# Kernel tuning notes

Hardware: AMD Instinct MI355X
Metric: run time of the kernel (lower is better)

The kernel has to match this reference:

```python
import jax, jax.numpy as jnp
from jax import lax
import numpy as np

B = 2
N_PER = 12000
TIMES = 16
C_IN = 4
# sparse_shape = grid_size[::-1] + [1,0,0], grid_size=[160,160,40]
S1 = (41, 160, 160)
S2 = (21, 80, 80)   # conv2: k3 s2 p1
S3 = (11, 40, 40)   # conv3: k3 s2 p1
S4 = (5, 20, 20)    # conv4: k3 s2 p(0,1,1)
SOUT = (2, 20, 20)  # conv_out: k(3,1,1) s(2,1,1) p0
# per-BN-layer channel counts, flattened into gamma/beta vectors
CH = [16, 16, 32, 32, 32, 64, 64, 64, 64, 64, 64, 128]
OFF = np.concatenate([[0], np.cumsum(CH)]).tolist()


def _downsample_coords(coords, in_shape, k, s, p):
    # spconv SparseConv3d output index rule: output j active iff some active
    # input x satisfies j*s - p <= x <= j*s - p + k - 1 within bounds.
    out_shape = np.array([(in_shape[i] + 2 * p[i] - k[i]) // s[i] + 1 for i in range(3)])
    b, xs = coords[:, :1], coords[:, 1:]
    s_arr = np.array(s)
    cand = []
    for o0 in range(k[0]):
        for o1 in range(k[1]):
            for o2 in range(k[2]):
                j = xs + np.array([p[0] - o0, p[1] - o1, p[2] - o2])
                ok = np.all(j % s_arr == 0, axis=1)
                jj = j // s_arr
                ok &= np.all((jj >= 0) & (jj < out_shape), axis=1)
                cand.append(np.concatenate([b[ok], jj[ok]], axis=1))
    return np.unique(np.concatenate(cand, axis=0), axis=0).astype(np.int32)


def _make_coords():
    rng = np.random.default_rng(0)
    ncell = S1[0] * S1[1] * S1[2]
    per = []
    for b in range(B):
        flat = rng.choice(ncell, size=N_PER, replace=False)
        z, y, x = np.unravel_index(flat, S1)
        per.append(np.stack([np.full(N_PER, b), z, y, x], axis=1))
    c1 = np.concatenate(per, axis=0).astype(np.int32)
    c2 = _downsample_coords(c1, S1, (3, 3, 3), (2, 2, 2), (1, 1, 1))
    c3 = _downsample_coords(c2, S2, (3, 3, 3), (2, 2, 2), (1, 1, 1))
    c4 = _downsample_coords(c3, S3, (3, 3, 3), (2, 2, 2), (0, 1, 1))
    c5 = _downsample_coords(c4, S4, (3, 1, 1), (2, 1, 1), (0, 0, 0))
    return c1, c2, c3, c4, c5


def _w(key, shape):
    fan_in = shape[0] * shape[1] * shape[2] * shape[3]
    return jax.random.normal(key, shape, jnp.float32) * np.float32(np.sqrt(2.0 / fan_in))


def setup_inputs():
    c1, c2, c3, c4, c5 = _make_coords()
    ks = jax.random.split(jax.random.key(0), 16)
    t = TIMES
    return {
        "voxel_features": jax.random.normal(ks[0], (c1.shape[0], C_IN), jnp.float32),
        "w_in": _w(ks[1], (3, 3, 3, C_IN, t)),
        "w1": _w(ks[2], (3, 3, 3, t, t)),
        "w2_0": _w(ks[3], (3, 3, 3, t, 2 * t)),
        "w2_1": _w(ks[4], (3, 3, 3, 2 * t, 2 * t)),
        "w2_2": _w(ks[5], (3, 3, 3, 2 * t, 2 * t)),
        "w3_0": _w(ks[6], (3, 3, 3, 2 * t, 4 * t)),
        "w3_1": _w(ks[7], (3, 3, 3, 4 * t, 4 * t)),
        "w3_2": _w(ks[8], (3, 3, 3, 4 * t, 4 * t)),
        "w4_0": _w(ks[9], (3, 3, 3, 4 * t, 4 * t)),
        "w4_1": _w(ks[10], (3, 3, 3, 4 * t, 4 * t)),
        "w4_2": _w(ks[11], (3, 3, 3, 4 * t, 4 * t)),
        "w_out": _w(ks[12], (3, 1, 1, 4 * t, 8 * t)),
        "gamma": 1.0 + 0.1 * jax.random.normal(ks[13], (sum(CH),), jnp.float32),
        "beta": 0.1 * jax.random.normal(ks[14], (sum(CH),), jnp.float32),
        "coords1": jnp.asarray(c1), "coords2": jnp.asarray(c2),
        "coords3": jnp.asarray(c3), "coords4": jnp.asarray(c4),
        "coords_out": jnp.asarray(c5),
    }


def _sp_conv(feats, in_coords, w, in_shape, out_coords, stride, padding):
    # spconv's rulebook gather->matmul->scatter over active sites computes the
    # same values as a dense conv on a zero-filled grid, read back only at the
    # active output coordinates (subm: out_coords == in_coords).
    dense = jnp.zeros((B,) + in_shape + (feats.shape[1],), feats.dtype)
    dense = dense.at[in_coords[:, 0], in_coords[:, 1], in_coords[:, 2], in_coords[:, 3]].set(feats)
    out = lax.conv_general_dilated(dense, w, window_strides=stride,
                                   padding=[(p, p) for p in padding],
                                   dimension_numbers=("NDHWC", "DHWIO", "NDHWC"))
    return out[out_coords[:, 0], out_coords[:, 1], out_coords[:, 2], out_coords[:, 3]]


def _bn_relu(x, g, b):
    # nn.BatchNorm1d(eps=1e-3) in training mode over the active voxels, + ReLU
    mu = jnp.mean(x, axis=0)
    var = jnp.mean(jnp.square(x - mu), axis=0)
    return jax.nn.relu((x - mu) * (g * lax.rsqrt(var + 1e-3)) + b)


def _forward(voxel_features, ws, gamma, beta, c1, c2, c3, c4, c5):
    layers = [
        (0, c1, S1, c1, (1, 1, 1), (1, 1, 1)),   # conv_input (subm, 4->16)
        (1, c1, S1, c1, (1, 1, 1), (1, 1, 1)),   # conv1 (subm)
        (2, c1, S1, c2, (2, 2, 2), (1, 1, 1)),   # conv2 spconv s2
        (3, c2, S2, c2, (1, 1, 1), (1, 1, 1)),
        (4, c2, S2, c2, (1, 1, 1), (1, 1, 1)),
        (5, c2, S2, c3, (2, 2, 2), (1, 1, 1)),   # conv3 spconv s2
        (6, c3, S3, c3, (1, 1, 1), (1, 1, 1)),
        (7, c3, S3, c3, (1, 1, 1), (1, 1, 1)),
        (8, c3, S3, c4, (2, 2, 2), (0, 1, 1)),   # conv4 spconv s2, pad (0,1,1)
        (9, c4, S4, c4, (1, 1, 1), (1, 1, 1)),
        (10, c4, S4, c4, (1, 1, 1), (1, 1, 1)),
        (11, c4, S4, c5, (2, 1, 1), (0, 0, 0)),  # conv_out k(3,1,1) s(2,1,1)
    ]
    x = voxel_features
    for i, ci, si, co, st, pd in layers:
        x = _sp_conv(x, ci, ws[i], si, co, st, pd)
        x = _bn_relu(x, gamma[OFF[i]:OFF[i + 1]], beta[OFF[i]:OFF[i + 1]])
    return x  # encoded_spconv_tensor features, [N_out, 8*times]


def reference(voxel_features, w_in, w1, w2_0, w2_1, w2_2, w3_0, w3_1, w3_2,
              w4_0, w4_1, w4_2, w_out, gamma, beta,
              coords1, coords2, coords3, coords4, coords_out):
    ws = [w_in, w1, w2_0, w2_1, w2_2, w3_0, w3_1, w3_2, w4_0, w4_1, w4_2, w_out]
    return _forward(voxel_features, ws, gamma, beta,
                    coords1, coords2, coords3, coords4, coords_out)
```

## Files before the change

kernel.cpp:

```cpp
#include <hip/hip_runtime.h>
#include <hip/hip_bf16.h>


typedef __attribute__((ext_vector_type(8))) short bf16x8;
typedef __attribute__((ext_vector_type(4))) short bf16x4s;
typedef __attribute__((ext_vector_type(4))) float f32x4;

typedef const __attribute__((address_space(1))) unsigned int* gas_ptr;
typedef __attribute__((address_space(3))) unsigned int* las_ptr;

__device__ __forceinline__ void dma16(const unsigned short* g, unsigned short* l) {
    __builtin_amdgcn_global_load_lds((gas_ptr)g, (las_ptr)l, 16, 0, 0);
}

__device__ inline unsigned short f2bf(float f) {
    unsigned u = __builtin_bit_cast(unsigned, f);
    u += 0x7FFFu + ((u >> 16) & 1u);
    return (unsigned short)(u >> 16);
}

struct ScatterArgs {
    const int* coords[4];
    int* grid[4];
    int n[4];
    int D[4], H[4], W[4];
};

__global__ __launch_bounds__(256) void scatter_grid_all(ScatterArgs a) {
    const int l = blockIdx.y;
    const int i = blockIdx.x * 256 + threadIdx.x;
    if (i >= a.n[l]) return;
    const int* c = a.coords[l] + 4 * i;
    a.grid[l][((c[0] * a.D[l] + c[1]) * a.H[l] + c[2]) * a.W[l] + c[3]] = i;
}

struct PrepArgs {
    const float* src[11];
    unsigned short* dst[11];
    int T[11], CIN[11], COUT[11], total[11];
};

__global__ __launch_bounds__(256) void prep_w_all(PrepArgs a) {
    const int l = blockIdx.y;
    const int i = blockIdx.x * 256 + threadIdx.x;
    if (i >= a.total[l]) return;
    const int COUT = a.COUT[l], CIN = a.CIN[l], T = a.T[l];
    const int co = i % COUT; const int r = i / COUT; const int ci = r % CIN; const int t = r / CIN;
    unsigned short v = (t < T) ? f2bf(a.src[l][i]) : (unsigned short)0;
    a.dst[l][((size_t)t * COUT + co) * CIN + ci] = v;
}

__global__ __launch_bounds__(256, 4) void sp_conv0(const float* __restrict__ fin,
                                                   const int* __restrict__ grid,
                                                   const int* __restrict__ oc, int n_out,
                                                   const float* __restrict__ w,
                                                   float* __restrict__ out,
                                                   int D, int H, int W) {
    const int c = threadIdx.x & 15;
    const int p = (blockIdx.x * 256 + threadIdx.x) >> 4;
    if (p >= n_out) return;
    const int b   = oc[4*p+0];
    const int iz0 = oc[4*p+1] - 1;
    const int iy0 = oc[4*p+2] - 1;
    const int ix0 = oc[4*p+3] - 1;
    const int* gb = grid + b * (D * H * W);
    float acc = 0.f;
    for (int kd = 0; kd < 3; ++kd) {
        const int iz = iz0 + kd;
        if ((unsigned)iz >= (unsigned)D) continue;
        for (int kh = 0; kh < 3; ++kh) {
            const int iy = iy0 + kh;
            if ((unsigned)iy >= (unsigned)H) continue;
            for (int kw = 0; kw < 3; ++kw) {
                const int ix = ix0 + kw;
                if ((unsigned)ix >= (unsigned)W) continue;
                const int idx = gb[(iz*H + iy)*W + ix];
                if (idx < 0) continue;
                const float4 v = *(const float4*)(fin + (size_t)idx * 4);
                const float* wp = w + (size_t)((kd*3 + kh)*3 + kw) * 64 + c;
                acc = fmaf(v.x, wp[0],  acc);
                acc = fmaf(v.y, wp[16], acc);
                acc = fmaf(v.z, wp[32], acc);
                acc = fmaf(v.w, wp[48], acc);
            }
        }
    }
    out[(size_t)p*16 + c] = acc;
}

template<int COUT, int BT>
__global__ __launch_bounds__(256, 4) void sp_conv_lds16(
    const unsigned short* __restrict__ fin, const int* __restrict__ grid,
    const int* __restrict__ oc, int n_out,
    const unsigned short* __restrict__ wt, float* __restrict__ out,
    float* __restrict__ stats,
    int D, int H, int W, int sz, int sy, int sx, int pz, int py, int px)
{
    constexpr int T  = 27;
    constexpr int NBATCH = (T + BT - 1)/BT;
    constexpr int TP = NBATCH*BT;
    constexpr int NT = COUT/16;
    constexpr int NB = (COUT == 16) ? BT/2 : BT;

    __shared__ unsigned short Abuf[4*BT*16*16];
    __shared__ unsigned short Bbuf[BT*COUT*16];
    __shared__ float ls[2*COUT];

    const int l     = threadIdx.x & 63;
    const int w     = threadIdx.x >> 6;
    const int n     = l & 15;
    const int quad  = l >> 4;
    const int pbase = blockIdx.x * 64 + w * 16;

    if (threadIdx.x < 2*COUT) ls[threadIdx.x] = 0.f;

    int idx[TP];
    if (quad == 0) {
        int pc = pbase + n;
        if (pc > n_out - 1) pc = n_out - 1;
        const int4 cc = ((const int4*)oc)[pc];
        const int* gb = grid + cc.x * (D * H * W);
        const int iz0 = cc.y * sz - pz;
        const int iy0 = cc.z * sy - py;
        const int ix0 = cc.w * sx - px;
#pragma unroll
        for (int tap = 0; tap < TP; ++tap) {
            const int te = tap < T ? tap : 0;
            const int kd = te/9, kr = te%9, kh = kr/3, kw = kr%3;
            const int iz = iz0 + kd, iy = iy0 + kh, ix = ix0 + kw;
            const bool ok = (tap < T) && (unsigned)iz < (unsigned)D &&
                            (unsigned)iy < (unsigned)H && (unsigned)ix < (unsigned)W;
            const int cz = iz < 0 ? 0 : (iz >= D ? D-1 : iz);
            const int cy = iy < 0 ? 0 : (iy >= H ? H-1 : iy);
            const int cx = ix < 0 ? 0 : (ix >= W ? W-1 : ix);
            const int g = gb[(cz*H + cy)*W + cx];
            idx[tap] = ok ? g : -1;
        }
    }

    f32x4 acc[NT];
#pragma unroll
    for (int t = 0; t < NT; ++t) acc[t] = (f32x4){0.f, 0.f, 0.f, 0.f};

    const int h  = l >> 5;
    const int m  = (l >> 1) & 15;
    const int ch = l & 1;

#pragma unroll
    for (int tb0 = 0; tb0 < TP; tb0 += BT) {
#pragma unroll
        for (int q = 0; q < BT/2; ++q) {
            const int v0 = __shfl(idx[tb0 + 2*q],     m);
            const int v1 = __shfl(idx[tb0 + 2*q + 1], m);
            const int row = h ? v1 : v0;
            const unsigned short* gp = fin + (ptrdiff_t)row*16 + ch*8;
            unsigned short* lp = Abuf + (w*BT + 2*q)*16*16;
            dma16(gp, lp);
        }
        for (int q = w; q < NB; q += 4) {
            if constexpr (COUT == 16) {
                const int tap = tb0 + 2*q + h;
                const int tw = tap < T ? tap : T;
                const unsigned short* gp = wt + ((size_t)tw*COUT + m)*16 + ch*8;
                unsigned short* lp = Bbuf + (2*q)*COUT*16;
                dma16(gp, lp);
            } else {
                const int tap = tb0 + q;
                const int tw = tap < T ? tap : T;
                const int r = l >> 1;
                const unsigned short* gp = wt + ((size_t)tw*COUT + r)*16 + ch*8;
                unsigned short* lp = Bbuf + q*COUT*16;
                dma16(gp, lp);
            }
        }
        __syncthreads();
#pragma unroll
        for (int jp = 0; jp < BT/2; ++jp) {
            const int ts = 2*jp + (quad >> 1);
            bf16x8 a = *(const bf16x8*)(Abuf + ((w*BT + ts)*16 + n)*16 + (quad & 1)*8);
#pragma unroll
            for (int t = 0; t < NT; ++t) {
                bf16x8 b = *(const bf16x8*)(Bbuf + (ts*COUT + t*16 + n)*16 + (quad & 1)*8);
                acc[t] = __builtin_amdgcn_mfma_f32_16x16x32_bf16(a, b, acc[t], 0, 0, 0);
            }
        }
        __syncthreads();
    }

#pragma unroll
    for (int t = 0; t < NT; ++t)
#pragma unroll
        for (int r = 0; r < 4; ++r) {
            const int p = pbase + quad*4 + r;
            if (p < n_out) out[(size_t)p * COUT + t*16 + n] = acc[t][r];
        }

#pragma unroll
    for (int t = 0; t < NT; ++t) {
        float s1 = 0.f, s2 = 0.f;
#pragma unroll
        for (int r = 0; r < 4; ++r) {
            const int p = pbase + quad*4 + r;
            if (p < n_out) { const float v = acc[t][r]; s1 += v; s2 += v*v; }
        }
        s1 += __shfl_xor(s1, 16); s2 += __shfl_xor(s2, 16);
        s1 += __shfl_xor(s1, 32); s2 += __shfl_xor(s2, 32);
        if (quad == 0) {
            atomicAdd(&ls[t*16 + n], s1);
            atomicAdd(&ls[COUT + t*16 + n], s2);
        }
    }
    __syncthreads();
    if (threadIdx.x < 2*COUT) atomicAdd(&stats[threadIdx.x], ls[threadIdx.x]);
}

template<int CIN, int COUT, int BT, int KD, int KH, int KW, int MB>
__global__ __launch_bounds__(256, MB) void sp_conv_lds(
    const unsigned short* __restrict__ fin, const int* __restrict__ grid,
    const int* __restrict__ oc, int n_out,
    const unsigned short* __restrict__ wt, float* __restrict__ out,
    float* __restrict__ stats,
    int D, int H, int W, int sz, int sy, int sx, int pz, int py, int px)
{
    constexpr int T    = KD*KH*KW;
    constexpr int NBATCH = (T + BT - 1)/BT;
    constexpr int TP   = NBATCH*BT;
    constexpr int NT   = COUT/16;
    constexpr int S    = CIN/32;
    constexpr int LPR  = CIN/8;
    constexpr int RPD  = 64/LPR;
    constexpr int ADMA = 16/RPD;
    constexpr int BDMA = COUT/RPD;

    __shared__ unsigned short Abuf[4*BT*16*CIN];
    __shared__ unsigned short Bbuf[BT*COUT*CIN];
    __shared__ float ls[2*COUT];

    const int l     = threadIdx.x & 63;
    const int w     = threadIdx.x >> 6;
    const int n     = l & 15;
    const int quad  = l >> 4;
    const int pbase = blockIdx.x * 64 + w * 16;

    if (threadIdx.x < 2*COUT) ls[threadIdx.x] = 0.f;

    int idx[TP];
    if (quad == 0) {
        int pc = pbase + n;
        if (pc > n_out - 1) pc = n_out - 1;
        const int4 cc = ((const int4*)oc)[pc];
        const int* gb = grid + cc.x * (D * H * W);
        const int iz0 = cc.y * sz - pz;
        const int iy0 = cc.z * sy - py;
        const int ix0 = cc.w * sx - px;
#pragma unroll
        for (int tap = 0; tap < TP; ++tap) {
            const int te = tap < T ? tap : 0;
            const int kd = te/(KH*KW), kr = te%(KH*KW), kh = kr/KW, kw = kr%KW;
            const int iz = iz0 + kd, iy = iy0 + kh, ix = ix0 + kw;
            const bool ok = (tap < T) && (unsigned)iz < (unsigned)D &&
                            (unsigned)iy < (unsigned)H && (unsigned)ix < (unsigned)W;
            const int cz = iz < 0 ? 0 : (iz >= D ? D-1 : iz);
            const int cy = iy < 0 ? 0 : (iy >= H ? H-1 : iy);
            const int cx = ix < 0 ? 0 : (ix >= W ? W-1 : ix);
            const int g = gb[(cz*H + cy)*W + cx];
            idx[tap] = ok ? g : -1;
        }
    }

    f32x4 acc[NT];
#pragma unroll
    for (int t = 0; t < NT; ++t) acc[t] = (f32x4){0.f, 0.f, 0.f, 0.f};

#pragma unroll
    for (int tb0 = 0; tb0 < TP; tb0 += BT) {
#pragma unroll
        for (int j = 0; j < BT; ++j) {
#pragma unroll
            for (int d = 0; d < ADMA; ++d) {
                const int m  = d*RPD + l/LPR;
                const int i0 = __shfl(idx[tb0+j], m);
                const int slot = (l % LPR) ^ (m % LPR);
                const unsigned short* gp = fin + (ptrdiff_t)i0*CIN + slot*8;
                unsigned short* lp = Abuf + ((w*BT + j)*16 + d*RPD)*CIN;
                dma16(gp, lp);
            }
        }
        for (int q = w; q < BT*BDMA; q += 4) {
            const int j = q / BDMA, d = q % BDMA;
            const int t = tb0 + j;
            const int tw = t < T ? t : T;
            const int r  = d*RPD + l/LPR;
            const int slot = (l % LPR) ^ (r % LPR);
            const unsigned short* gp = wt + ((size_t)tw*COUT + r)*CIN + slot*8;
            unsigned short* lp = Bbuf + (j*COUT + d*RPD)*CIN;
            dma16(gp, lp);
        }
        __syncthreads();
#pragma unroll
        for (int j = 0; j < BT; ++j) {
            const unsigned short* Aw = Abuf + (w*BT + j)*16*CIN;
            const unsigned short* Bw = Bbuf + j*COUT*CIN;
#pragma unroll
            for (int s = 0; s < S; ++s) {
                const int c = s*4 + quad;
                bf16x8 a = *(const bf16x8*)(Aw + n*CIN + ((c ^ (n % LPR)) * 8));
#pragma unroll
                for (int t = 0; t < NT; ++t) {
                    const int r = t*16 + n;
                    bf16x8 b = *(const bf16x8*)(Bw + r*CIN + ((c ^ (r % LPR)) * 8));
                    acc[t] = __builtin_amdgcn_mfma_f32_16x16x32_bf16(a, b, acc[t], 0, 0, 0);
                }
            }
        }
        __syncthreads();
    }

#pragma unroll
    for (int t = 0; t < NT; ++t)
#pragma unroll
        for (int r = 0; r < 4; ++r) {
            const int p = pbase + quad*4 + r;
            if (p < n_out) out[(size_t)p * COUT + t*16 + n] = acc[t][r];
        }

#pragma unroll
    for (int t = 0; t < NT; ++t) {
        float s1 = 0.f, s2 = 0.f;
#pragma unroll
        for (int r = 0; r < 4; ++r) {
            const int p = pbase + quad*4 + r;
            if (p < n_out) { const float v = acc[t][r]; s1 += v; s2 += v*v; }
        }
        s1 += __shfl_xor(s1, 16); s2 += __shfl_xor(s2, 16);
        s1 += __shfl_xor(s1, 32); s2 += __shfl_xor(s2, 32);
        if (quad == 0) {
            atomicAdd(&ls[t*16 + n], s1);
            atomicAdd(&ls[COUT + t*16 + n], s2);
        }
    }
    __syncthreads();
    if (threadIdx.x < 2*COUT) atomicAdd(&stats[threadIdx.x], ls[threadIdx.x]);
}

template<int C>
__global__ __launch_bounds__(256) void reduce_stats(const float* __restrict__ x, int nn,
                                                    float* __restrict__ stats)
{
    constexpr int R = 256 / C;
    __shared__ float s1[256];
    __shared__ float s2[256];
    const int c = threadIdx.x % C;
    const int r = threadIdx.x / C;
    float a1 = 0.f, a2 = 0.f;
    for (int i = blockIdx.x * R + r; i < nn; i += R * gridDim.x) {
        float v = x[(size_t)i*C + c];
        a1 += v;
        a2 += v * v;
    }
    s1[threadIdx.x] = a1;
    s2[threadIdx.x] = a2;
    __syncthreads();
    for (int off = 128; off >= C; off >>= 1) {
        if (threadIdx.x < off) {
            s1[threadIdx.x] += s1[threadIdx.x + off];
            s2[threadIdx.x] += s2[threadIdx.x + off];
        }
        __syncthreads();
    }
    if (threadIdx.x < C) {
        atomicAdd(&stats[c],     s1[threadIdx.x]);
        atomicAdd(&stats[C + c], s2[threadIdx.x]);
    }
}

__device__ inline void stv4(float* p, float4 v) { *(float4*)p = v; }
__device__ inline void stv4(unsigned short* p, float4 v) {
    bf16x4s o;
    o.x = (short)f2bf(v.x); o.y = (short)f2bf(v.y);
    o.z = (short)f2bf(v.z); o.w = (short)f2bf(v.w);
    *(bf16x4s*)p = o;
}

template<int C, typename OUT>
__global__ __launch_bounds__(256) void bn_relu_apply(const float* __restrict__ x,
                                                     OUT* __restrict__ y, int nn,
                                                     const float* __restrict__ stats,
                                                     const float* __restrict__ gamma,
                                                     const float* __restrict__ beta)
{
    const size_t q = (size_t)blockIdx.x * blockDim.x + threadIdx.x;
    if (q >= (size_t)nn * (C/4)) return;
    const int c = (int)(q % (size_t)(C/4)) * 4;
    const float inv_n = 1.f / (float)nn;
    const float4 xv = *(const float4*)(x + q*4);
    const float4 s1 = *(const float4*)(stats + c);
    const float4 s2 = *(const float4*)(stats + C + c);
    const float4 gm = *(const float4*)(gamma + c);
    const float4 bt = *(const float4*)(beta + c);
    float4 o;
    { float mu=s1.x*inv_n, var=s2.x*inv_n-mu*mu, g=gm.x*rsqrtf(var+1e-3f);
      float v=(xv.x-mu)*g+bt.x; o.x = v>0.f? v:0.f; }
    { float mu=s1.y*inv_n, var=s2.y*inv_n-mu*mu, g=gm.y*rsqrtf(var+1e-3f);
      float v=(xv.y-mu)*g+bt.y; o.y = v>0.f? v:0.f; }
    { float mu=s1.z*inv_n, var=s2.z*inv_n-mu*mu, g=gm.z*rsqrtf(var+1e-3f);
      float v=(xv.z-mu)*g+bt.z; o.z = v>0.f? v:0.f; }
    { float mu=s1.w*inv_n, var=s2.w*inv_n-mu*mu, g=gm.w*rsqrtf(var+1e-3f);
      float v=(xv.w-mu)*g+bt.w; o.w = v>0.f? v:0.f; }
    stv4(y + q*4, o);
}

extern "C" void kernel_launch(void* const* d_in, const int* in_sizes, int n_in,
                              void* d_out, int out_size, void* d_ws, size_t ws_size,
                              hipStream_t stream) {
    const float* WPTR[12] = {
        (const float*)d_in[1], (const float*)d_in[2], (const float*)d_in[3],
        (const float*)d_in[4], (const float*)d_in[5], (const float*)d_in[6],
        (const float*)d_in[7], (const float*)d_in[8], (const float*)d_in[9],
        (const float*)d_in[10], (const float*)d_in[11], (const float*)d_in[12] };
    const float* vf    = (const float*)d_in[0];
    const float* gamma = (const float*)d_in[13];
    const float* beta  = (const float*)d_in[14];
    const int* c1 = (const int*)d_in[15];
    const int* c2 = (const int*)d_in[16];
    const int* c3 = (const int*)d_in[17];
    const int* c4 = (const int*)d_in[18];
    const int* c5 = (const int*)d_in[19];
    const int N1 = in_sizes[15] / 4;
    const int N2 = in_sizes[16] / 4;
    const int N3 = in_sizes[17] / 4;
    const int N4 = in_sizes[18] / 4;
    const int N5 = in_sizes[19] / 4;

    static const int LT[12]  = {27,27,27,27,27,27,27,27,27,27,27,3};
    static const int LCI[12] = {4,16,16,32,32,32,64,64,64,64,64,64};
    static const int LCO[12] = {16,16,32,32,32,64,64,64,64,64,64,128};

    const size_t G1 = (size_t)2*41*160*160;
    const size_t G2 = (size_t)2*21*80*80;
    const size_t G3 = (size_t)2*11*40*40;
    const size_t G4 = (size_t)2*5*20*20;
    int* grid1 = (int*)d_ws;
    int* grid2 = grid1 + G1;
    int* grid3 = grid2 + G2;
    int* grid4 = grid3 + G3;
    float* stats = (float*)(grid4 + G4);

    size_t maxE = (size_t)N1*16;
    if ((size_t)N2*32  > maxE) maxE = (size_t)N2*32;
    if ((size_t)N3*64  > maxE) maxE = (size_t)N3*64;
    if ((size_t)N4*64  > maxE) maxE = (size_t)N4*64;
    if ((size_t)N5*128 > maxE) maxE = (size_t)N5*128;
    maxE = (maxE + 7) & ~(size_t)7;

    float* raw = stats + 12*256;
    unsigned short* padA = (unsigned short*)(raw + maxE);
    unsigned short* fA   = padA + 128;
    unsigned short* padB = fA + maxE;
    unsigned short* fB   = padB + 128;
    unsigned short* wtb  = fB + maxE;
    size_t wtoff[12];
    {
        size_t o = 0;
        for (int i = 1; i < 12; ++i) {
            wtoff[i] = o;
            o += (size_t)(LT[i] + 1) * LCI[i] * LCO[i];
        }
    }

    hipMemsetAsync(grid1, 0xFF, (G1+G2+G3+G4)*sizeof(int), stream);
    hipMemsetAsync(stats, 0, 12*256*sizeof(float), stream);
    hipMemsetAsync(padA, 0, 128*sizeof(unsigned short), stream);
    hipMemsetAsync(padB, 0, 128*sizeof(unsigned short), stream);

    {
        ScatterArgs sa;
        sa.coords[0]=c1; sa.coords[1]=c2; sa.coords[2]=c3; sa.coords[3]=c4;
        sa.grid[0]=grid1; sa.grid[1]=grid2; sa.grid[2]=grid3; sa.grid[3]=grid4;
        sa.n[0]=N1; sa.n[1]=N2; sa.n[2]=N3; sa.n[3]=N4;
        sa.D[0]=41; sa.H[0]=160; sa.W[0]=160;
        sa.D[1]=21; sa.H[1]= 80; sa.W[1]= 80;
        sa.D[2]=11; sa.H[2]= 40; sa.W[2]= 40;
        sa.D[3]= 5; sa.H[3]= 20; sa.W[3]= 20;
        int mx = N1; if (N2>mx) mx=N2; if (N3>mx) mx=N3; if (N4>mx) mx=N4;
        dim3 g((mx + 255)/256, 4);
        scatter_grid_all<<<g, 256, 0, stream>>>(sa);
    }
    {
        PrepArgs pa;
        int mx = 0;
        for (int i = 1; i < 12; ++i) {
            pa.src[i-1] = WPTR[i];
            pa.dst[i-1] = wtb + wtoff[i];
            pa.T[i-1] = LT[i]; pa.CIN[i-1] = LCI[i]; pa.COUT[i-1] = LCO[i];
            pa.total[i-1] = (LT[i]+1)*LCI[i]*LCO[i];
            if (pa.total[i-1] > mx) mx = pa.total[i-1];
        }
        dim3 g((mx + 255)/256, 11);
        prep_w_all<<<g, 256, 0, stream>>>(pa);
    }

    enum { GOFF_0 = 0, GOFF_1 = 16, GOFF_2 = 32, GOFF_3 = 64, GOFF_4 = 96, GOFF_5 = 128,
           GOFF_6 = 192, GOFF_7 = 256, GOFF_8 = 320, GOFF_9 = 384, GOFF_10 = 448, GOFF_11 = 512 };

#define APPLY(i, COUT, NP, FOUT_T, FOUT) \
    bn_relu_apply<COUT, FOUT_T><<<(((size_t)(NP)*(COUT)/4) + 255)/256, 256, 0, stream>>>( \
        raw, FOUT, NP, stats + (i)*256, gamma + GOFF_##i, beta + GOFF_##i);

    sp_conv0<<<((size_t)N1*16 + 255)/256, 256, 0, stream>>>(vf, grid1, c1, N1, WPTR[0], raw, 41,160,160);
    { int rb = (N1 + 15)/16; if (rb > 240) rb = 240;
      reduce_stats<16><<<rb, 256, 0, stream>>>(raw, N1, stats + 0*256); }
    APPLY(0, 16, N1, unsigned short, fA);

#define CONVS(i, COUT, BT, FIN, GRD, OC, NP, D,H,W, SZ,SY,SX, PZ,PY,PX) \
    sp_conv_lds16<COUT,BT><<<((NP)+63)/64, 256, 0, stream>>>( \
        FIN, GRD, OC, NP, wtb + wtoff[i], raw, stats + (i)*256, D,H,W, SZ,SY,SX, PZ,PY,PX);

#define CONVL(i, CIN, COUT, BT, MB, KD,KH,KW, FIN, GRD, OC, NP, D,H,W, SZ,SY,SX, PZ,PY,PX) \
    sp_conv_lds<CIN,COUT,BT,KD,KH,KW,MB><<<((NP)+63)/64, 256, 0, stream>>>( \
        FIN, GRD, OC, NP, wtb + wtoff[i], raw, stats + (i)*256, D,H,W, SZ,SY,SX, PZ,PY,PX);

    CONVS( 1, 16, 10,   fA, grid1, c1, N1, 41,160,160, 1,1,1, 1,1,1); APPLY( 1, 16, N1, unsigned short, fB);
    CONVS( 2, 32, 10,   fB, grid1, c2, N2, 41,160,160, 2,2,2, 1,1,1); APPLY( 2, 32, N2, unsigned short, fA);
    CONVL ( 3, 32, 32, 9, 2, 3,3,3, fA, grid2, c2, N2, 21, 80, 80, 1,1,1, 1,1,1); APPLY( 3, 32, N2, unsigned short, fB);
    CONVL ( 4, 32, 32, 9, 2, 3,3,3, fB, grid2, c2, N2, 21, 80, 80, 1,1,1, 1,1,1); APPLY( 4, 32, N2, unsigned short, fA);
    CONVL ( 5, 32, 64, 9, 2, 3,3,3, fA, grid2, c3, N3, 21, 80, 80, 2,2,2, 1,1,1); APPLY( 5, 64, N3, unsigned short, fB);
    CONVL ( 6, 64, 64, 9, 1, 3,3,3, fB, grid3, c3, N3, 11, 40, 40, 1,1,1, 1,1,1); APPLY( 6, 64, N3, unsigned short, fA);
    CONVL ( 7, 64, 64, 9, 1, 3,3,3, fA, grid3, c3, N3, 11, 40, 40, 1,1,1, 1,1,1); APPLY( 7, 64, N3, unsigned short, fB);
    CONVL ( 8, 64, 64, 9, 1, 3,3,3, fB, grid3, c4, N4, 11, 40, 40, 2,2,2, 0,1,1); APPLY( 8, 64, N4, unsigned short, fA);
    CONVL ( 9, 64, 64, 9, 1, 3,3,3, fA, grid4, c4, N4,  5, 20, 20, 1,1,1, 1,1,1); APPLY( 9, 64, N4, unsigned short, fB);
    CONVL (10, 64, 64, 9, 1, 3,3,3, fB, grid4, c4, N4,  5, 20, 20, 1,1,1, 1,1,1); APPLY(10, 64, N4, unsigned short, fA);
    CONVL (11, 64,128, 3, 2, 3,1,1, fA, grid4, c5, N5,  5, 20, 20, 2,1,1, 0,0,0); APPLY(11, 128, N5, float, (float*)d_out);
#undef CONVS
#undef CONVL
#undef APPLY
}
```

Measured before the change: 431.2 us.

## Run submanifold convs as dense tiled convolutions over a scattered bf16 grid

Adds a dense-grid path for the stride-1 submanifold convolutions at levels 2-4. BN+ReLU now scatters activations into a zeroed dense bf16 volume. A new kernel then loads a haloed 3D tile into LDS and runs all 27 taps as MFMAs on contiguous rows, writing results only at active sites. This replaces the per-voxel gather through the index grid with regular tile loads. The cost is extra memsets of the dense volume and wasted MFMA work on empty cells, which is significant given how sparse the levels are.

```diff
diff --git a/kernel.cpp b/kernel.cpp
--- a/kernel.cpp
+++ b/kernel.cpp
@@ -343,6 +343,158 @@
     if (threadIdx.x < 2*COUT) atomicAdd(&stats[threadIdx.x], ls[threadIdx.x]);
 }
 
+template<int C, int TZ, int TY, int TX, int BTW>
+__global__ __launch_bounds__(256, 1) void sp_conv_dense(
+    const unsigned short* __restrict__ dense, const int* __restrict__ grid,
+    const unsigned short* __restrict__ wt, float* __restrict__ out,
+    float* __restrict__ stats, const unsigned short* __restrict__ zrow,
+    int D, int H, int W, int ZTn, int YTn, int XTn)
+{
+    constexpr int T   = 27;
+    constexpr int HZ = TZ+2, HY = TY+2, HX = TX+2;
+    constexpr int R   = HZ*HY*HX;
+    constexpr int LPR = C/8;
+    constexpr int RPD = 64/LPR;
+    constexpr int RPI = 4*RPD;
+    constexpr int NDMA = (R + RPI - 1)/RPI;
+    constexpr int RPAD = NDMA*RPI;
+    constexpr int M   = TZ*TY*TX;
+    constexpr int WPW = M/4;
+    constexpr int MT  = WPW/16;
+    constexpr int NT  = C/16;
+    constexpr int S   = C/32;
+    constexpr int BDMA = C/RPD;
+
+    __shared__ unsigned short Hbuf[RPAD*C];
+    __shared__ unsigned short Bbuf[BTW*C*C];
+    __shared__ float ls[2*C];
+
+    const int l    = threadIdx.x & 63;
+    const int w    = threadIdx.x >> 6;
+    const int n    = l & 15;
+    const int quad = l >> 4;
+
+    int r1 = blockIdx.x;
+    const int xt = r1 % XTn; r1 /= XTn;
+    const int yt = r1 % YTn; r1 /= YTn;
+    const int zt = r1 % ZTn; r1 /= ZTn;
+    const int b  = r1;
+    const int z0 = zt*TZ, y0 = yt*TY, x0 = xt*TX;
+    const int* gb = grid + b * (D*H*W);
+    const size_t dbase = (size_t)b * D*H*W;
+
+    if (threadIdx.x < 2*C) ls[threadIdx.x] = 0.f;
+
+#pragma unroll
+    for (int d = 0; d < NDMA; ++d) {
+        const int r0  = (d*4 + w)*RPD;
+        const int row = r0 + l/LPR;
+        const int slot = (l % LPR) ^ (row % LPR);
+        const unsigned short* gp;
+        if (row < R) {
+            const int hz = row/(HY*HX);
+            const int hy = (row/HX) % HY;
+            const int hx = row % HX;
+            const int gz = z0 - 1 + hz, gy = y0 - 1 + hy, gx = x0 - 1 + hx;
+            const bool ok = (unsigned)gz < (unsigned)D && (unsigned)gy < (unsigned)H &&
+                            (unsigned)gx < (unsigned)W;
+            gp = ok ? dense + (dbase + (size_t)(gz*H + gy)*W + gx)*C + slot*8
+                    : zrow + (l % LPR)*8;
+        } else {
+            gp = zrow + (l % LPR)*8;
+        }
+        dma16(gp, Hbuf + r0*C);
+    }
+
+    int prow[MT];
+#pragma unroll
+    for (int mt = 0; mt < MT; ++mt) {
+        const int pos = w*WPW + mt*16 + n;
+        const int dz = pos/(TY*TX), dy = (pos/TX)%TY, dx = pos%TX;
+        prow[mt] = dz*(HY*HX) + dy*HX + dx;
+    }
+
+    f32x4 acc[MT][NT];
+#pragma unroll
+    for (int mt = 0; mt < MT; ++mt)
+#pragma unroll
+        for (int t = 0; t < NT; ++t) acc[mt][t] = (f32x4){0.f, 0.f, 0.f, 0.f};
+
+#pragma unroll
+    for (int batch = 0; batch < (T + BTW - 1)/BTW; ++batch) {
+        const int tb0 = batch*BTW;
+        const int nb  = (tb0 + BTW <= T) ? BTW : T - tb0;
+        for (int q = w; q < nb*BDMA; q += 4) {
+            const int j = q / BDMA, d = q % BDMA;
+            const int tap = tb0 + j;
+            const int rr  = d*RPD + l/LPR;
+            const int slot = (l % LPR) ^ (rr % LPR);
+            dma16(wt + ((size_t)tap*C + rr)*C + slot*8, Bbuf + (j*C + d*RPD)*C);
+        }
+        __syncthreads();
+#pragma unroll
+        for (int j = 0; j < nb; ++j) {
+            const int tap = tb0 + j;
+            const int kd = tap/9, kh = (tap/3)%3, kw = tap%3;
+            const int toff = kd*(HY*HX) + kh*HX + kw;
+#pragma unroll
+            for (int s = 0; s < S; ++s) {
+                const int c = s*4 + quad;
+                bf16x8 bfr[NT];
+#pragma unroll
+                for (int t = 0; t < NT; ++t) {
+                    const int rr = t*16 + n;
+                    bfr[t] = *(const bf16x8*)(Bbuf + (j*C + rr)*C + ((c ^ (rr & (LPR-1)))*8));
+                }
+#pragma unroll
+                for (int mt = 0; mt < MT; ++mt) {
+                    const int arow = prow[mt] + toff;
+                    bf16x8 a = *(const bf16x8*)(Hbuf + arow*C + ((c ^ (arow & (LPR-1)))*8));
+#pragma unroll
+                    for (int t = 0; t < NT; ++t)
+                        acc[mt][t] = __builtin_amdgcn_mfma_f32_16x16x32_bf16(a, bfr[t], acc[mt][t], 0, 0, 0);
+                }
+            }
+        }
+        __syncthreads();
+    }
+
+    float s1[NT], s2[NT];
+#pragma unroll
+    for (int t = 0; t < NT; ++t) { s1[t] = 0.f; s2[t] = 0.f; }
+#pragma unroll
+    for (int mt = 0; mt < MT; ++mt) {
+#pragma unroll
+        for (int r = 0; r < 4; ++r) {
+            const int pos = w*WPW + mt*16 + quad*4 + r;
+            const int dz = pos/(TY*TX), dy = (pos/TX)%TY, dx = pos%TX;
+            const int gz = z0 + dz, gy = y0 + dy, gx = x0 + dx;
+            int p = -1;
+            if (gz < D && gy < H && gx < W) p = gb[(gz*H + gy)*W + gx];
+            if (p >= 0) {
+#pragma unroll
+                for (int t = 0; t < NT; ++t) {
+                    const float v = acc[mt][t][r];
+                    out[(size_t)p*C + t*16 + n] = v;
+                    s1[t] += v; s2[t] += v*v;
+                }
+            }
+        }
+    }
+#pragma unroll
+    for (int t = 0; t < NT; ++t) {
+        float a1 = s1[t], a2 = s2[t];
+        a1 += __shfl_xor(a1, 16); a2 += __shfl_xor(a2, 16);
+        a1 += __shfl_xor(a1, 32); a2 += __shfl_xor(a2, 32);
+        if (quad == 0) {
+            atomicAdd(&ls[t*16 + n], a1);
+            atomicAdd(&ls[C + t*16 + n], a2);
+        }
+    }
+    __syncthreads();
+    if (threadIdx.x < 2*C) atomicAdd(&stats[threadIdx.x], ls[threadIdx.x]);
+}
+
 template<int C>
 __global__ __launch_bounds__(256) void reduce_stats(const float* __restrict__ x, int nn,
                                                     float* __restrict__ stats)
@@ -382,6 +534,20 @@
     *(bf16x4s*)p = o;
 }
 
+__device__ inline float4 bn_math(float4 xv, float4 s1, float4 s2, float4 gm, float4 bt,
+                                 float inv_n) {
+    float4 o;
+    { float mu=s1.x*inv_n, var=s2.x*inv_n-mu*mu, g=gm.x*rsqrtf(var+1e-3f);
+      float v=(xv.x-mu)*g+bt.x; o.x = v>0.f? v:0.f; }
+    { float mu=s1.y*inv_n, var=s2.y*inv_n-mu*mu, g=gm.y*rsqrtf(var+1e-3f);
+      float v=(xv.y-mu)*g+bt.y; o.y = v>0.f? v:0.f; }
+    { float mu=s1.z*inv_n, var=s2.z*inv_n-mu*mu, g=gm.z*rsqrtf(var+1e-3f);
+      float v=(xv.z-mu)*g+bt.z; o.z = v>0.f? v:0.f; }
+    { float mu=s1.w*inv_n, var=s2.w*inv_n-mu*mu, g=gm.w*rsqrtf(var+1e-3f);
+      float v=(xv.w-mu)*g+bt.w; o.w = v>0.f? v:0.f; }
+    return o;
+}
+
 template<int C, typename OUT>
 __global__ __launch_bounds__(256) void bn_relu_apply(const float* __restrict__ x,
                                                      OUT* __restrict__ y, int nn,
@@ -392,22 +558,34 @@
     const size_t q = (size_t)blockIdx.x * blockDim.x + threadIdx.x;
     if (q >= (size_t)nn * (C/4)) return;
     const int c = (int)(q % (size_t)(C/4)) * 4;
-    const float inv_n = 1.f / (float)nn;
-    const float4 xv = *(const float4*)(x + q*4);
-    const float4 s1 = *(const float4*)(stats + c);
-    const float4 s2 = *(const float4*)(stats + C + c);
-    const float4 gm = *(const float4*)(gamma + c);
-    const float4 bt = *(const float4*)(beta + c);
-    float4 o;
-    { float mu=s1.x*inv_n, var=s2.x*inv_n-mu*mu, g=gm.x*rsqrtf(var+1e-3f);
-      float v=(xv.x-mu)*g+bt.x; o.x = v>0.f? v:0.f; }
-    { float mu=s1.y*inv_n, var=s2.y*inv_n-mu*mu, g=gm.y*rsqrtf(var+1e-3f);
-      float v=(xv.y-mu)*g+bt.y; o.y = v>0.f? v:0.f; }
-    { float mu=s1.z*inv_n, var=s2.z*inv_n-mu*mu, g=gm.z*rsqrtf(var+1e-3f);
-      float v=(xv.z-mu)*g+bt.z; o.z = v>0.f? v:0.f; }
-    { float mu=s1.w*inv_n, var=s2.w*inv_n-mu*mu, g=gm.w*rsqrtf(var+1e-3f);
-      float v=(xv.w-mu)*g+bt.w; o.w = v>0.f? v:0.f; }
+    const float4 o = bn_math(*(const float4*)(x + q*4),
+                             *(const float4*)(stats + c), *(const float4*)(stats + C + c),
+                             *(const float4*)(gamma + c), *(const float4*)(beta + c),
+                             1.f / (float)nn);
     stv4(y + q*4, o);
+}
+
+template<int C>
+__global__ __launch_bounds__(256) void bn_relu_apply_dense(const float* __restrict__ x,
+                                                           unsigned short* __restrict__ dense,
+                                                           int nn,
+                                                           const float* __restrict__ stats,
+                                                           const float* __restrict__ gamma,
+                                                           const float* __restrict__ beta,
+                                                           const int* __restrict__ coords,
+                                                           int D, int H, int W)
+{
+    const size_t q = (size_t)blockIdx.x * blockDim.x + threadIdx.x;
+    if (q >= (size_t)nn * (C/4)) return;
+    const int c = (int)(q % (size_t)(C/4)) * 4;
+    const int p = (int)(q / (size_t)(C/4));
+    const float4 o = bn_math(*(const float4*)(x + q*4),
+                             *(const float4*)(stats + c), *(const float4*)(stats + C + c),
+                             *(const float4*)(gamma + c), *(const float4*)(beta + c),
+                             1.f / (float)nn);
+    const int4 cc = ((const int4*)coords)[p];
+    const size_t cell = ((size_t)((cc.x*D + cc.y)*H + cc.z)*W + cc.w);
+    stv4(dense + cell*C + c, o);
 }
 
 extern "C" void kernel_launch(void* const* d_in, const int* in_sizes, int n_in,
@@ -460,13 +638,16 @@
     unsigned short* fB   = padB + 128;
     unsigned short* wtb  = fB + maxE;
     size_t wtoff[12];
+    size_t wtot = 0;
     {
         size_t o = 0;
         for (int i = 1; i < 12; ++i) {
             wtoff[i] = o;
             o += (size_t)(LT[i] + 1) * LCI[i] * LCO[i];
         }
-    }
+        wtot = (o + 15) & ~(size_t)15;
+    }
+    unsigned short* dbuf = wtb + wtot;
 
     hipMemsetAsync(grid1, 0xFF, (G1+G2+G3+G4)*sizeof(int), stream);
     hipMemsetAsync(stats, 0, 12*256*sizeof(float), stream);
@@ -507,6 +688,11 @@
     bn_relu_apply<COUT, FOUT_T><<<(((size_t)(NP)*(COUT)/4) + 255)/256, 256, 0, stream>>>( \
         raw, FOUT, NP, stats + (i)*256, gamma + GOFF_##i, beta + GOFF_##i);
 
+#define APPLYD(i, C, NP, CC, D,H,W) \
+    hipMemsetAsync(dbuf, 0, (size_t)2*(D)*(H)*(W)*(C)*2, stream); \
+    bn_relu_apply_dense<C><<<(((size_t)(NP)*(C)/4) + 255)/256, 256, 0, stream>>>( \
+        raw, dbuf, NP, stats + (i)*256, gamma + GOFF_##i, beta + GOFF_##i, CC, D,H,W);
+
     sp_conv0<<<((size_t)N1*16 + 255)/256, 256, 0, stream>>>(vf, grid1, c1, N1, WPTR[0], raw, 41,160,160);
     { int rb = (N1 + 15)/16; if (rb > 240) rb = 240;
       reduce_stats<16><<<rb, 256, 0, stream>>>(raw, N1, stats + 0*256); }
@@ -520,18 +706,25 @@
     sp_conv_lds<CIN,COUT,BT,KD,KH,KW,MB><<<((NP)+63)/64, 256, 0, stream>>>( \
         FIN, GRD, OC, NP, wtb + wtoff[i], raw, stats + (i)*256, D,H,W, SZ,SY,SX, PZ,PY,PX);
 
+#define CONVD(i, C, TZ,TY,TX, BTW, GRD, D,H,W) \
+    { const int zt = ((D)+(TZ)-1)/(TZ), yt = ((H)+(TY)-1)/(TY), xt = ((W)+(TX)-1)/(TX); \
+      sp_conv_dense<C,TZ,TY,TX,BTW><<<2*zt*yt*xt, 256, 0, stream>>>( \
+          dbuf, GRD, wtb + wtoff[i], raw, stats + (i)*256, padA, D,H,W, zt,yt,xt); }
+
     CONVS( 1, 16, 10,   fA, grid1, c1, N1, 41,160,160, 1,1,1, 1,1,1); APPLY( 1, 16, N1, unsigned short, fB);
-    CONVS( 2, 32, 10,   fB, grid1, c2, N2, 41,160,160, 2,2,2, 1,1,1); APPLY( 2, 32, N2, unsigned short, fA);
-    CONVL ( 3, 32, 32, 9, 2, 3,3,3, fA, grid2, c2, N2, 21, 80, 80, 1,1,1, 1,1,1); APPLY( 3, 32, N2, unsigned short, fB);
-    CONVL ( 4, 32, 32, 9, 2, 3,3,3, fB, grid2, c2, N2, 21, 80, 80, 1,1,1, 1,1,1); APPLY( 4, 32, N2, unsigned short, fA);
-    CONVL ( 5, 32, 64, 9, 2, 3,3,3, fA, grid2, c3, N3, 21, 80, 80, 2,2,2, 1,1,1); APPLY( 5, 64, N3, unsigned short, fB);
-    CONVL ( 6, 64, 64, 9, 1, 3,3,3, fB, grid3, c3, N3, 11, 40, 40, 1,1,1, 1,1,1); APPLY( 6, 64, N3, unsigned short, fA);
-    CONVL ( 7, 64, 64, 9, 1, 3,3,3, fA, grid3, c3, N3, 11, 40, 40, 1,1,1, 1,1,1); APPLY( 7, 64, N3, unsigned short, fB);
-    CONVL ( 8, 64, 64, 9, 1, 3,3,3, fB, grid3, c4, N4, 11, 40, 40, 2,2,2, 0,1,1); APPLY( 8, 64, N4, unsigned short, fA);
-    CONVL ( 9, 64, 64, 9, 1, 3,3,3, fA, grid4, c4, N4,  5, 20, 20, 1,1,1, 1,1,1); APPLY( 9, 64, N4, unsigned short, fB);
-    CONVL (10, 64, 64, 9, 1, 3,3,3, fB, grid4, c4, N4,  5, 20, 20, 1,1,1, 1,1,1); APPLY(10, 64, N4, unsigned short, fA);
-    CONVL (11, 64,128, 3, 2, 3,1,1, fA, grid4, c5, N5,  5, 20, 20, 2,1,1, 0,0,0); APPLY(11, 128, N5, float, (float*)d_out);
+    CONVS( 2, 32, 10,   fB, grid1, c2, N2, 41,160,160, 2,2,2, 1,1,1); APPLYD( 2, 32, N2, c2, 21,80,80);
+    CONVD( 3, 32, 4,8,16, 27, grid2, 21,80,80);                       APPLYD( 3, 32, N2, c2, 21,80,80);
+    CONVD( 4, 32, 4,8,16, 27, grid2, 21,80,80);                       APPLY( 4, 32, N2, unsigned short, fA);
+    CONVL( 5, 32, 64, 9, 2, 3,3,3, fA, grid2, c3, N3, 21,80,80, 2,2,2, 1,1,1); APPLYD( 5, 64, N3, c3, 11,40,40);
+    CONVD( 6, 64, 4,4,8, 10, grid3, 11,40,40);                        APPLYD( 6, 64, N3, c3, 11,40,40);
+    CONVD( 7, 64, 4,4,8, 10, grid3, 11,40,40);                        APPLY( 7, 64, N3, unsigned short, fB);
+    CONVL( 8, 64, 64, 9, 1, 3,3,3, fB, grid3, c4, N4, 11,40,40, 2,2,2, 0,1,1); APPLYD( 8, 64, N4, c4, 5,20,20);
+    CONVD( 9, 64, 4,4,8, 10, grid4, 5,20,20);                         APPLYD( 9, 64, N4, c4, 5,20,20);
+    CONVD(10, 64, 4,4,8, 10, grid4, 5,20,20);                         APPLY(10, 64, N4, unsigned short, fA);
+    CONVL(11, 64,128, 3, 2, 3,1,1, fA, grid4, c5, N5,  5,20,20, 2,1,1, 0,0,0); APPLY(11, 128, N5, float, (float*)d_out);
 #undef CONVS
 #undef CONVL
+#undef CONVD
 #undef APPLY
-}
+#undef APPLYD
+}
```

Measured after the change: 462.7 us. 1.07x slower.
